# Performance work log

Hardware: AMD Instinct MI355X
Metric: run time of the kernel (lower is better)

Reference implementation:

```python
import jax, jax.numpy as jnp
import numpy as np

R = 131072          # total proposals (ROIs)
D = 1024            # input feature dim (ShapeSpec.channels)
NUM_CLASSES = 80    # COCO foreground classes
REID_DIM = 256      # reid_feat_dim
BOX_DIM = 4


def setup_inputs() -> dict:
    key = jax.random.key(0)
    ks = jax.random.split(key, 12)
    x = jax.random.normal(ks[0], (R, D), dtype=jnp.float32)
    # cls_score: Linear(D, num_classes+1), init std=0.01, bias 0
    W_cls = 0.01 * jax.random.normal(ks[1], (NUM_CLASSES + 1, D), dtype=jnp.float32)
    b_cls = jnp.zeros((NUM_CLASSES + 1,), dtype=jnp.float32)
    # bbox_pred: Linear(D, num_classes * 4), init std=0.001, bias 0
    W_bbox = 0.001 * jax.random.normal(ks[2], (NUM_CLASSES * BOX_DIM, D), dtype=jnp.float32)
    b_bbox = jnp.zeros((NUM_CLASSES * BOX_DIM,), dtype=jnp.float32)
    # reid_embed_head: MLP(D, 256, 256, 3) -> Linear(D,256), Linear(256,256), Linear(256,256)
    def lin(k, fan_in, fan_out):
        kw, kb = jax.random.split(k)
        bound = 1.0 / np.sqrt(fan_in)
        W = jax.random.uniform(kw, (fan_out, fan_in), minval=-bound, maxval=bound, dtype=jnp.float32)
        b = jax.random.uniform(kb, (fan_out,), minval=-bound, maxval=bound, dtype=jnp.float32)
        return W, b
    W1, b1 = lin(ks[3], D, REID_DIM)
    W2, b2 = lin(ks[4], REID_DIM, REID_DIM)
    W3, b3 = lin(ks[5], REID_DIM, REID_DIM)
    return {"x": x, "W_cls": W_cls, "b_cls": b_cls, "W_bbox": W_bbox, "b_bbox": b_bbox,
            "W1": W1, "b1": b1, "W2": W2, "b2": b2, "W3": W3, "b3": b3}


def reference(x, W_cls, b_cls, W_bbox, b_bbox, W1, b1, W2, b2, W3, b3):
    # x: [R, D] (already flat; torch forward flattens if dim > 2)
    scores = x @ W_cls.T + b_cls                 # [R, K+1]
    proposal_deltas = x @ W_bbox.T + b_bbox      # [R, K*4]
    # MLP with ReLU on all but last layer
    h = jax.nn.relu(x @ W1.T + b1)               # [R, 256]
    h = jax.nn.relu(h @ W2.T + b2)               # [R, 256]
    embeds = h @ W3.T + b3                       # [R, 256]
    return scores, proposal_deltas, embeds
```

## Files before the change

### kernel.cpp

```cpp
#include <hip/hip_runtime.h>
#include <hip/hip_bf16.h>
#include <stdint.h>

#define R_TOT   131072
#define D_IN    1024
#define N_CLS   81
#define N_BOX   320
#define N_H     256
#define N1_USED 657
#define N1_PAD  672
#define NB_COLS 336

typedef __attribute__((ext_vector_type(8))) short short8;
typedef __attribute__((ext_vector_type(4))) float f32x4;

__device__ __forceinline__ unsigned short f2bf(float f) {
  union { float f; unsigned u; } v; v.f = f;
  unsigned r = v.u + 0x7FFFu + ((v.u >> 16) & 1u);
  return (unsigned short)(r >> 16);
}

__device__ __forceinline__ short8 cvt8(float4 a, float4 b) {
  short8 v;
  v[0] = (short)f2bf(a.x); v[1] = (short)f2bf(a.y);
  v[2] = (short)f2bf(a.z); v[3] = (short)f2bf(a.w);
  v[4] = (short)f2bf(b.x); v[5] = (short)f2bf(b.y);
  v[6] = (short)f2bf(b.z); v[7] = (short)f2bf(b.w);
  return v;
}

__device__ __forceinline__ void async_lds16(void* lds, const void* g) {
  __builtin_amdgcn_global_load_lds(
      (const __attribute__((address_space(1))) unsigned int*)g,
      (__attribute__((address_space(3))) unsigned int*)lds, 16, 0, 0);
}

__global__ void prep_w1(const float* __restrict__ Wc, const float* __restrict__ Wb,
                        const float* __restrict__ W1, unsigned short* __restrict__ Wp)
{
  int idx = blockIdx.x * 256 + threadIdx.x;
  int p   = idx / (N1_PAD * 32);
  int rem = idx % (N1_PAD * 32);
  int n   = rem >> 5;
  int kk  = rem & 31;
  int k   = p * 32 + kk;
  float w = 0.f;
  if (n < N_CLS)               w = Wc[(size_t)n * D_IN + k];
  else if (n < N_CLS + N_BOX)  w = Wb[(size_t)(n - N_CLS) * D_IN + k];
  else if (n < N1_USED)        w = W1[(size_t)(n - (N_CLS + N_BOX)) * D_IN + k];
  Wp[idx] = f2bf(w);
}

__global__ void prep_w23(const float* __restrict__ W2, const float* __restrict__ W3,
                         unsigned short* __restrict__ W2b, unsigned short* __restrict__ W3b)
{
  int idx = blockIdx.x * 256 + threadIdx.x;
  if (idx < 65536) W2b[idx] = f2bf(W2[idx]);
  else             W3b[idx - 65536] = f2bf(W3[idx - 65536]);
}

__global__ __launch_bounds__(448, 6) void g1_kernel(
    const float* __restrict__ x, const unsigned short* __restrict__ Wp,
    const float* __restrict__ b_cls, const float* __restrict__ b_box,
    const float* __restrict__ b1,
    float* __restrict__ scores, float* __restrict__ deltas,
    unsigned short* __restrict__ h1)
{
  __shared__ __attribute__((aligned(16))) unsigned short As[2][64 * 32];
  __shared__ __attribute__((aligned(16))) unsigned short Bs[2][NB_COLS * 32];

  const int tid  = threadIdx.x;
  const int wave = tid >> 6;
  const int lane = tid & 63;
  const int orig  = blockIdx.x;
  const int work  = (orig & 7) * 512 + (orig >> 3);
  const int m0    = (work >> 1) * 64;
  const int nbase = (work & 1) * NB_COLS;

  f32x4 acc[4][3];
#pragma unroll
  for (int i = 0; i < 4; ++i)
#pragma unroll
    for (int j = 0; j < 3; ++j)
      acc[i][j] = (f32x4){0.f, 0.f, 0.f, 0.f};

  {
    const unsigned short* wsrc = Wp + (size_t)nbase * 32;
#pragma unroll
    for (int i = 0; i < 3; ++i) {
      int chunk = tid + i * 448;
      async_lds16((char*)&Bs[0][0] + chunk * 16, (const char*)wsrc + chunk * 16);
    }
    if (tid < 256) {
      int row = tid >> 2, kq = tid & 3;
      const float* src = x + (size_t)(m0 + row) * D_IN + kq * 8;
      float4 f0 = *(const float4*)src;
      float4 f1 = *(const float4*)(src + 4);
      *(short8*)&As[0][row * 32 + kq * 8] = cvt8(f0, f1);
    }
  }
  __syncthreads();

  const int lr = lane & 15;
  const int lk = (lane >> 4) * 8;

  for (int kp = 0; kp < 32; ++kp) {
    const int cur = kp & 1;
    const int nxt = cur ^ 1;
    const bool last = (kp == 31);

    float4 fa0, fa1;
    if (!last) {
      if (tid < 256) {
        int row = tid >> 2, kq = tid & 3;
        const float* src = x + (size_t)(m0 + row) * D_IN + (size_t)(kp + 1) * 32 + kq * 8;
        fa0 = *(const float4*)src;
        fa1 = *(const float4*)(src + 4);
      }
      const unsigned short* wsrc = Wp + (size_t)(kp + 1) * (N1_PAD * 32) + (size_t)nbase * 32;
#pragma unroll
      for (int i = 0; i < 3; ++i) {
        int chunk = tid + i * 448;
        async_lds16((char*)&Bs[nxt][0] + chunk * 16, (const char*)wsrc + chunk * 16);
      }
    }

    short8 af[4], bfr[3];
#pragma unroll
    for (int mi = 0; mi < 4; ++mi)
      af[mi] = *(const short8*)&As[cur][(mi * 16 + lr) * 32 + lk];
#pragma unroll
    for (int ni = 0; ni < 3; ++ni)
      bfr[ni] = *(const short8*)&Bs[cur][(wave * 48 + ni * 16 + lr) * 32 + lk];
#pragma unroll
    for (int mi = 0; mi < 4; ++mi)
#pragma unroll
      for (int ni = 0; ni < 3; ++ni)
        acc[mi][ni] = __builtin_amdgcn_mfma_f32_16x16x32_bf16(af[mi], bfr[ni], acc[mi][ni], 0, 0, 0);

    if (!last && tid < 256) {
      int row = tid >> 2, kq = tid & 3;
      *(short8*)&As[nxt][row * 32 + kq * 8] = cvt8(fa0, fa1);
    }
    __syncthreads();
  }

  const int rbase = m0 + ((lane >> 4) << 2);
#pragma unroll
  for (int mi = 0; mi < 4; ++mi) {
#pragma unroll
    for (int ni = 0; ni < 3; ++ni) {
      int n = nbase + wave * 48 + ni * 16 + lr;
      if (n >= N1_USED) continue;
      if (n < N_CLS) {
        float bb = b_cls[n];
#pragma unroll
        for (int j = 0; j < 4; ++j) {
          int r = rbase + mi * 16 + j;
          scores[(size_t)r * N_CLS + n] = acc[mi][ni][j] + bb;
        }
      } else if (n < N_CLS + N_BOX) {
        int nb = n - N_CLS;
        float bb = b_box[nb];
#pragma unroll
        for (int j = 0; j < 4; ++j) {
          int r = rbase + mi * 16 + j;
          deltas[(size_t)r * N_BOX + nb] = acc[mi][ni][j] + bb;
        }
      } else {
        int nh = n - (N_CLS + N_BOX);
        float bb = b1[nh];
#pragma unroll
        for (int j = 0; j < 4; ++j) {
          int r = rbase + mi * 16 + j;
          float h = acc[mi][ni][j] + bb;
          h1[(size_t)r * N_H + nh] = f2bf(fmaxf(h, 0.f));
        }
      }
    }
  }
}

__device__ __forceinline__ void g23_stage(unsigned short* Asb, unsigned short* Bsb,
    const unsigned short* __restrict__ A, const unsigned short* __restrict__ Bw,
    int m0, int kp, int tid)
{
  {
    int row = tid >> 2, kq = tid & 3;
    async_lds16((char*)Asb + tid * 16,
                (const char*)(A + (size_t)(m0 + row) * N_H + (size_t)kp * 32 + kq * 8));
  }
#pragma unroll
  for (int i = 0; i < 2; ++i) {
    int chunk = tid + i * 512;
    int row = chunk >> 2, kq = chunk & 3;
    async_lds16((char*)Bsb + chunk * 16,
                (const char*)(Bw + (size_t)row * N_H + (size_t)kp * 32 + kq * 8));
  }
}

template <int RELU, int OUT_BF16>
__global__ __launch_bounds__(512, 1) void g23_kernel(
    const unsigned short* __restrict__ A, const unsigned short* __restrict__ Bw,
    const float* __restrict__ bias, void* __restrict__ outv)
{
  __shared__ __attribute__((aligned(16))) unsigned short As[2][128 * 32];
  __shared__ __attribute__((aligned(16))) unsigned short Bs[2][256 * 32];
  const int tid  = threadIdx.x;
  const int wave = tid >> 6, lane = tid & 63;
  const int wm = wave >> 2, wn = wave & 3;
  const int m0 = blockIdx.x * 128;

  f32x4 acc[4][4];
#pragma unroll
  for (int i = 0; i < 4; ++i)
#pragma unroll
    for (int j = 0; j < 4; ++j)
      acc[i][j] = (f32x4){0.f, 0.f, 0.f, 0.f};

  g23_stage(&As[0][0], &Bs[0][0], A, Bw, m0, 0, tid);
  __syncthreads();

  const int lr = lane & 15;
  const int lk = (lane >> 4) * 8;

  for (int kp = 0; kp < 8; ++kp) {
    const int cur = kp & 1, nxt = cur ^ 1;
    if (kp < 7) g23_stage(&As[nxt][0], &Bs[nxt][0], A, Bw, m0, kp + 1, tid);

    short8 af[4], bfr[4];
#pragma unroll
    for (int mi = 0; mi < 4; ++mi)
      af[mi] = *(const short8*)&As[cur][(wm * 64 + mi * 16 + lr) * 32 + lk];
#pragma unroll
    for (int ni = 0; ni < 4; ++ni)
      bfr[ni] = *(const short8*)&Bs[cur][(wn * 64 + ni * 16 + lr) * 32 + lk];
#pragma unroll
    for (int mi = 0; mi < 4; ++mi)
#pragma unroll
      for (int ni = 0; ni < 4; ++ni)
        acc[mi][ni] = __builtin_amdgcn_mfma_f32_16x16x32_bf16(af[mi], bfr[ni], acc[mi][ni], 0, 0, 0);
    __syncthreads();
  }

#pragma unroll
  for (int mi = 0; mi < 4; ++mi) {
#pragma unroll
    for (int ni = 0; ni < 4; ++ni) {
      int n = wn * 64 + ni * 16 + lr;
      float bb = bias[n];
#pragma unroll
      for (int j = 0; j < 4; ++j) {
        int r = m0 + wm * 64 + mi * 16 + ((lane >> 4) << 2) + j;
        float v = acc[mi][ni][j] + bb;
        if (RELU) v = fmaxf(v, 0.f);
        if (OUT_BF16) ((unsigned short*)outv)[(size_t)r * N_H + n] = f2bf(v);
        else          ((float*)outv)[(size_t)r * N_H + n] = v;
      }
    }
  }
}

extern "C" void kernel_launch(void* const* d_in, const int* in_sizes, int n_in,
                              void* d_out, int out_size, void* d_ws, size_t ws_size,
                              hipStream_t stream)
{
  const float* x     = (const float*)d_in[0];
  const float* W_cls = (const float*)d_in[1];
  const float* b_cls = (const float*)d_in[2];
  const float* W_box = (const float*)d_in[3];
  const float* b_box = (const float*)d_in[4];
  const float* W1    = (const float*)d_in[5];
  const float* b1    = (const float*)d_in[6];
  const float* W2    = (const float*)d_in[7];
  const float* b2    = (const float*)d_in[8];
  const float* W3    = (const float*)d_in[9];
  const float* b3    = (const float*)d_in[10];

  float* scores = (float*)d_out;
  float* deltas = scores + (size_t)R_TOT * N_CLS;
  float* embeds = deltas + (size_t)R_TOT * N_BOX;

  char* ws = (char*)d_ws;
  unsigned short* Wp  = (unsigned short*)ws;
  unsigned short* W2b = (unsigned short*)(ws + 1376256);
  unsigned short* W3b = (unsigned short*)(ws + 1376256 + 131072);
  unsigned short* h   = (unsigned short*)(ws + 1638400);

  hipLaunchKernelGGL(prep_w1, dim3(2688), dim3(256), 0, stream, W_cls, W_box, W1, Wp);
  hipLaunchKernelGGL(prep_w23, dim3(512), dim3(256), 0, stream, W2, W3, W2b, W3b);
  hipLaunchKernelGGL(g1_kernel, dim3(4096), dim3(448), 0, stream,
                     x, Wp, b_cls, b_box, b1, scores, deltas, h);
  hipLaunchKernelGGL((g23_kernel<1, 1>), dim3(R_TOT / 128), dim3(512), 0, stream,
                     h, W2b, b2, (void*)h);
  hipLaunchKernelGGL((g23_kernel<0, 0>), dim3(R_TOT / 128), dim3(512), 0, stream,
                     h, W3b, b3, (void*)embeds);
}
```

Measured before the change: 452.1 us.

## Stage fp32 activations into LDS asynchronously and convert to bf16 at fragment load

The activation tile is now brought in through async global-to-LDS copies as fp32, alongside the weight tile, instead of being loaded into registers, converted in software and stored to LDS. The bf16 conversion moves to the fragment read using the hardware packed convert instruction. The intent is to remove the register staging and the costly software rounding from the main loop. In exchange the A tile doubles its LDS footprint and every wave repeats the conversion work. The launch-bounds occupancy hint is also dropped.

```diff
diff --git a/kernel.cpp b/kernel.cpp
--- a/kernel.cpp
+++ b/kernel.cpp
@@ -18,15 +18,6 @@
   union { float f; unsigned u; } v; v.f = f;
   unsigned r = v.u + 0x7FFFu + ((v.u >> 16) & 1u);
   return (unsigned short)(r >> 16);
-}
-
-__device__ __forceinline__ short8 cvt8(float4 a, float4 b) {
-  short8 v;
-  v[0] = (short)f2bf(a.x); v[1] = (short)f2bf(a.y);
-  v[2] = (short)f2bf(a.z); v[3] = (short)f2bf(a.w);
-  v[4] = (short)f2bf(b.x); v[5] = (short)f2bf(b.y);
-  v[6] = (short)f2bf(b.z); v[7] = (short)f2bf(b.w);
-  return v;
 }
 
 __device__ __forceinline__ void async_lds16(void* lds, const void* g) {
@@ -59,15 +50,15 @@
   else             W3b[idx - 65536] = f2bf(W3[idx - 65536]);
 }
 
-__global__ __launch_bounds__(448, 6) void g1_kernel(
+__global__ __launch_bounds__(448) void g1_kernel(
     const float* __restrict__ x, const unsigned short* __restrict__ Wp,
     const float* __restrict__ b_cls, const float* __restrict__ b_box,
     const float* __restrict__ b1,
     float* __restrict__ scores, float* __restrict__ deltas,
     unsigned short* __restrict__ h1)
 {
-  __shared__ __attribute__((aligned(16))) unsigned short As[2][64 * 32];
   __shared__ __attribute__((aligned(16))) unsigned short Bs[2][NB_COLS * 32];
+  __shared__ __attribute__((aligned(16))) float          As[2][64 * 32];
 
   const int tid  = threadIdx.x;
   const int wave = tid >> 6;
@@ -84,64 +75,56 @@
     for (int j = 0; j < 3; ++j)
       acc[i][j] = (f32x4){0.f, 0.f, 0.f, 0.f};
 
-  {
-    const unsigned short* wsrc = Wp + (size_t)nbase * 32;
-#pragma unroll
-    for (int i = 0; i < 3; ++i) {
-      int chunk = tid + i * 448;
-      async_lds16((char*)&Bs[0][0] + chunk * 16, (const char*)wsrc + chunk * 16);
-    }
-    if (tid < 256) {
-      int row = tid >> 2, kq = tid & 3;
-      const float* src = x + (size_t)(m0 + row) * D_IN + kq * 8;
-      float4 f0 = *(const float4*)src;
-      float4 f1 = *(const float4*)(src + 4);
-      *(short8*)&As[0][row * 32 + kq * 8] = cvt8(f0, f1);
-    }
-  }
+  auto stage = [&](int buf, int kp) {
+    const unsigned short* wsrc = Wp + (size_t)kp * (N1_PAD * 32) + (size_t)nbase * 32;
+#pragma unroll
+    for (int i = 0; i < 5; ++i) {
+      int c = tid + i * 448;
+      if (c < 1344) {
+        async_lds16((char*)&Bs[buf][0] + c * 16, (const char*)wsrc + c * 16);
+      } else if (c < 1856) {
+        int a = c - 1344;
+        int row = a >> 3, q = a & 7;
+        async_lds16((char*)&As[buf][0] + a * 16,
+                    (const char*)(x + (size_t)(m0 + row) * D_IN + (size_t)kp * 32 + q * 4));
+      }
+    }
+  };
+
+  stage(0, 0);
   __syncthreads();
 
   const int lr = lane & 15;
-  const int lk = (lane >> 4) * 8;
+  const int g2 = (lane >> 4) * 8;
+
+  union U8 { unsigned u[4]; short8 s; };
 
   for (int kp = 0; kp < 32; ++kp) {
     const int cur = kp & 1;
-    const int nxt = cur ^ 1;
-    const bool last = (kp == 31);
-
-    float4 fa0, fa1;
-    if (!last) {
-      if (tid < 256) {
-        int row = tid >> 2, kq = tid & 3;
-        const float* src = x + (size_t)(m0 + row) * D_IN + (size_t)(kp + 1) * 32 + kq * 8;
-        fa0 = *(const float4*)src;
-        fa1 = *(const float4*)(src + 4);
-      }
-      const unsigned short* wsrc = Wp + (size_t)(kp + 1) * (N1_PAD * 32) + (size_t)nbase * 32;
-#pragma unroll
-      for (int i = 0; i < 3; ++i) {
-        int chunk = tid + i * 448;
-        async_lds16((char*)&Bs[nxt][0] + chunk * 16, (const char*)wsrc + chunk * 16);
-      }
-    }
+    if (kp < 31) stage(cur ^ 1, kp + 1);
 
     short8 af[4], bfr[3];
 #pragma unroll
-    for (int mi = 0; mi < 4; ++mi)
-      af[mi] = *(const short8*)&As[cur][(mi * 16 + lr) * 32 + lk];
+    for (int mi = 0; mi < 4; ++mi) {
+      const float* base = &As[cur][(mi * 16 + lr) * 32 + g2];
+      float4 p0 = *(const float4*)base;
+      float4 p1 = *(const float4*)(base + 4);
+      U8 t;
+      asm("v_cvt_pk_bf16_f32 %0, %1, %2" : "=v"(t.u[0]) : "v"(p0.x), "v"(p0.y));
+      asm("v_cvt_pk_bf16_f32 %0, %1, %2" : "=v"(t.u[1]) : "v"(p0.z), "v"(p0.w));
+      asm("v_cvt_pk_bf16_f32 %0, %1, %2" : "=v"(t.u[2]) : "v"(p1.x), "v"(p1.y));
+      asm("v_cvt_pk_bf16_f32 %0, %1, %2" : "=v"(t.u[3]) : "v"(p1.z), "v"(p1.w));
+      af[mi] = t.s;
+    }
 #pragma unroll
     for (int ni = 0; ni < 3; ++ni)
-      bfr[ni] = *(const short8*)&Bs[cur][(wave * 48 + ni * 16 + lr) * 32 + lk];
+      bfr[ni] = *(const short8*)&Bs[cur][(wave * 48 + ni * 16 + lr) * 32 + g2];
 #pragma unroll
     for (int mi = 0; mi < 4; ++mi)
 #pragma unroll
       for (int ni = 0; ni < 3; ++ni)
         acc[mi][ni] = __builtin_amdgcn_mfma_f32_16x16x32_bf16(af[mi], bfr[ni], acc[mi][ni], 0, 0, 0);
 
-    if (!last && tid < 256) {
-      int row = tid >> 2, kq = tid & 3;
-      *(short8*)&As[nxt][row * 32 + kq * 8] = cvt8(fa0, fa1);
-    }
     __syncthreads();
   }
 
```

New measurement: 527.0 us. 1.17x slower.
